# Optimization experiments

Hardware: AMD Instinct MI355X
Metric: run time of the kernel (lower is better)

The kernel has to match this reference:

```python
import jax, jax.numpy as jnp
import numpy as np

B, T, N, IN, H, K = 8, 10, 50, 6, 256, 4
E = N * (N - 1)


def setup_inputs() -> dict:
    key = jax.random.key(0)
    ks = jax.random.split(key, 22)
    p = lambda k, shape: jax.random.normal(k, shape, jnp.float32) * 0.05
    return {
        "inputs": jax.random.normal(ks[0], (B, T, N, IN), jnp.float32),
        "sampled_edges": jax.random.uniform(ks[1], (B, T, E, K), dtype=jnp.float32),
        "msg_w1": p(ks[2], (K, H, 2 * H)), "msg_b1": p(ks[3], (K, H)),
        "msg_w2": p(ks[4], (K, H, H)), "msg_b2": p(ks[5], (K, H)),
        "w_hr": p(ks[6], (H, H)), "w_hi": p(ks[7], (H, H)), "w_hh": p(ks[8], (H, H)),
        "w_ir": p(ks[9], (H, IN)), "b_ir": p(ks[10], (H,)),
        "w_ii": p(ks[11], (H, IN)), "b_ii": p(ks[12], (H,)),
        "w_in": p(ks[13], (H, IN)), "b_in": p(ks[14], (H,)),
        "w_o1": p(ks[15], (H, H)), "b_o1": p(ks[16], (H,)),
        "w_o2": p(ks[17], (H, H)), "b_o2": p(ks[18], (H,)),
        "w_o3": p(ks[19], (IN, H)), "b_o3": p(ks[20], (IN,)),
    }


def reference(inputs, sampled_edges, msg_w1, msg_b1, msg_w2, msg_b2,
              w_hr, w_hi, w_hh, w_ir, b_ir, w_ii, b_ii, w_in, b_in,
              w_o1, b_o1, w_o2, b_o2, w_o3, b_o3):
    b, t, n, _ = inputs.shape
    k = msg_w1.shape[0]
    h = msg_w1.shape[1]
    # fully-connected directed graph, no self loops (static indices)
    send_np, recv_np = np.where(np.ones((n, n)) - np.eye(n))
    send = jnp.asarray(send_np)
    recv = jnp.asarray(recv_np)
    norm = float(k) - 1.0  # skip_first_edge_type = True

    def single_step(ins, rel, hidden):
        # ins: [B,N,IN], rel: [B,E,K], hidden: [B,N,H]
        pre = jnp.concatenate([hidden[:, recv], hidden[:, send]], axis=-1)  # [B,E,2H]
        all_msgs = jnp.zeros((b, pre.shape[1], h), inputs.dtype)
        for i in range(1, k):  # skip first edge type
            m = jnp.tanh(jnp.einsum('bef,hf->beh', pre, msg_w1[i]) + msg_b1[i])
            m = jnp.tanh(jnp.einsum('beh,jh->bej', m, msg_w2[i]) + msg_b2[i])
            all_msgs = all_msgs + m * rel[:, :, i:i + 1] / norm
        # scatter-add messages to receiver nodes (replaces onehot matmul)
        agg = jnp.zeros((b, n, h), inputs.dtype).at[:, recv].add(all_msgs) / (n - 1)
        r = jax.nn.sigmoid(ins @ w_ir.T + b_ir + agg @ w_hr.T)
        ig = jax.nn.sigmoid(ins @ w_ii.T + b_ii + agg @ w_hi.T)
        nn_ = jnp.tanh(ins @ w_in.T + b_in + r * (agg @ w_hh.T))
        hidden = (1 - ig) * nn_ + ig * hidden
        pred = jax.nn.relu(hidden @ w_o1.T + b_o1)
        pred = jax.nn.relu(pred @ w_o2.T + b_o2)
        pred = ins + (pred @ w_o3.T + b_o3)
        return pred, hidden

    x_t = jnp.swapaxes(inputs, 0, 1)         # [T,B,N,IN]
    e_t = jnp.swapaxes(sampled_edges, 0, 1)  # [T,B,E,K]
    h0 = jnp.zeros((b, n, h), inputs.dtype)

    def step(carry, xs):
        hidden, prev = carry
        xt, et, s = xs
        ins = jnp.where(s == 0, xt, prev)  # teacher_forcing=False: only step 0 uses inputs
        pred, hidden = single_step(ins, et, hidden)
        return (hidden, pred), pred

    _, preds = jax.lax.scan(step, (h0, jnp.zeros_like(x_t[0])), (x_t, e_t, jnp.arange(t)))
    return jnp.swapaxes(preds, 0, 1)  # [B,T,N,IN]
```

## Files before the change

### kernel.cpp

```cpp
#include <hip/hip_runtime.h>
#include <hip/hip_bf16.h>
#include <stdint.h>

#define B_ 8
#define T_ 10
#define N_ 50
#define IN_ 6
#define H_ 256
#define K_ 4
#define E_ 2450
#define ROWS 400
#define AP 102400

typedef __attribute__((ext_vector_type(8))) __bf16 bf16x8;
typedef __attribute__((ext_vector_type(4))) float f32x4;

__device__ __forceinline__ unsigned short f2bf(float x) {
    unsigned int u = __float_as_uint(x);
    u = (u + 0x7fffu + ((u >> 16) & 1u)) >> 16;
    return (unsigned short)u;
}
__device__ __forceinline__ unsigned pk2(float a, float b) {
    return (unsigned)f2bf(a) | ((unsigned)f2bf(b) << 16);
}
__device__ __forceinline__ float rcp_fast(float x) { return __builtin_amdgcn_rcpf(x); }
__device__ __forceinline__ float tanh_fast(float x) {
    float e = __expf(2.0f * x);
    return 1.0f - 2.0f * rcp_fast(e + 1.0f);
}
__device__ __forceinline__ float sigmoid_fast(float x) {
    return rcp_fast(1.0f + __expf(-x));
}

__global__ __launch_bounds__(256) void swizzle_weights(
        const float* __restrict__ w1, const float* __restrict__ w2,
        const float* __restrict__ whr, const float* __restrict__ whi,
        const float* __restrict__ whh, const float* __restrict__ wo1,
        const float* __restrict__ wo2,
        unsigned short* __restrict__ w1s, unsigned short* __restrict__ w2s,
        unsigned short* __restrict__ gws, unsigned short* __restrict__ wos,
        unsigned int* __restrict__ zero_region) {
    const int W1N = 3 * 16 * 16 * 64 * 8;
    const int W2N = 3 * 16 * 8 * 64 * 8;
    const int GWN = 3 * 65536;
    const int WON = 2 * 65536;
    int idx = blockIdx.x * 256 + threadIdx.x;
    if (idx < W1N) {
        int j = idx & 7, L = (idx >> 3) & 63, kt = (idx >> 9) & 15;
        int nt = (idx >> 13) & 15, i = idx >> 17;
        int n = nt * 16 + (L & 15);
        int k = kt * 32 + ((L >> 4) << 3) + j;
        w1s[idx] = f2bf(w1[((size_t)(i + 1) * H_ + n) * (2 * H_) + k]);
    } else if (idx < W1N + W2N) {
        int t = idx - W1N;
        int j = t & 7, L = (t >> 3) & 63, kt = (t >> 9) & 7;
        int nt = (t >> 12) & 15, i = t >> 16;
        int n = nt * 16 + (L & 15);
        int k = kt * 32 + ((L >> 4) << 3) + j;
        w2s[t] = f2bf(w2[((size_t)(i + 1) * H_ + n) * H_ + k]);
    } else if (idx < W1N + W2N + GWN) {
        int t = idx - (W1N + W2N);
        int j = t & 7, L = (t >> 3) & 63, kt = (t >> 9) & 7;
        int nt = (t >> 12) & 15, mat = t >> 16;
        int n = nt * 16 + (L & 15);
        int k = kt * 32 + ((L >> 4) << 3) + j;
        const float* src = (mat == 0) ? whr : (mat == 1) ? whi : whh;
        gws[t] = f2bf(src[(size_t)n * H_ + k]);
    } else if (idx < W1N + W2N + GWN + WON) {
        int t = idx - (W1N + W2N + GWN);
        int j = t & 7, L = (t >> 3) & 63, kt = (t >> 9) & 7;
        int nt = (t >> 12) & 15, g = t >> 16;
        int n = nt * 16 + (L & 15);
        int k = kt * 32 + ((L >> 4) << 3) + j;
        const float* src = (g == 0) ? wo1 : wo2;
        wos[t] = f2bf(src[(size_t)n * H_ + k]);
    } else {
        int t = idx - (W1N + W2N + GWN + WON);
        if (t < 153600) zero_region[t] = 0u;
    }
}

__global__ __launch_bounds__(256) void uv_kernel(
        const unsigned short* __restrict__ hb, const unsigned short* __restrict__ w1s,
        const float* __restrict__ b1, float* __restrict__ UV) {
    int mm = blockIdx.x / 6;
    int tyh = blockIdx.x % 6;
    int ty = tyh >> 1, half = tyh & 1;
    int lane = threadIdx.x & 63, wid = threadIdx.x >> 6;
    int col = lane & 15, q = lane >> 4;
    const bf16x8* w1f = (const bf16x8*)w1s;

    f32x4 acc[4];
    #pragma unroll
    for (int u = 0; u < 4; ++u) acc[u] = (f32x4){0.f, 0.f, 0.f, 0.f};
    #pragma unroll
    for (int kt = 0; kt < 8; ++kt) {
        bf16x8 a = *(const bf16x8*)&hb[(size_t)(mm * 16 + col) * H_ + kt * 32 + q * 8];
        #pragma unroll
        for (int u = 0; u < 4; ++u) {
            bf16x8 w = w1f[(size_t)((ty * 16 + wid * 4 + u) * 16 + half * 8 + kt) * 64 + lane];
            acc[u] = __builtin_amdgcn_mfma_f32_16x16x32_bf16(a, w, acc[u], 0, 0, 0);
        }
    }
    #pragma unroll
    for (int u = 0; u < 4; ++u) {
        float bias = (half == 0) ? b1[(ty + 1) * H_ + (wid * 4 + u) * 16 + col] : 0.0f;
        #pragma unroll
        for (int r = 0; r < 4; ++r)
            UV[((size_t)(mm * 16 + q * 4 + r) * 3 + ty) * 512 + half * 256 +
               (wid * 4 + u) * 16 + col] = acc[u][r] + bias;
    }
}

__global__ __launch_bounds__(256, 4) void msgagg_kernel(
        const float* __restrict__ UV, const float* __restrict__ edges,
        const unsigned short* __restrict__ w2s,
        const float* __restrict__ b2, float* __restrict__ aggP, int t) {
    __shared__ unsigned short m1F[32 * 512];
    __shared__ float relS[64];

    int ty = blockIdx.x / 400;
    int rem = blockIdx.x - ty * 400;
    int b = rem / 50;
    int r = rem - b * 50;
    int tid = threadIdx.x;
    int lane = tid & 63, wid = tid >> 6;
    int col = lane & 15, q = lane >> 4;

    if (tid < 64) {
        float v = 0.0f;
        if (tid < 50 && tid != r) {
            int e = tid * 49 + (r > tid ? r - 1 : r);
            v = edges[(((size_t)b * T_ + t) * E_ + e) * K_ + ty + 1];
        }
        relS[tid] = v;
    }

    {
        int row = wid * 16 + col;
        int sv = row < N_ ? row : N_ - 1;
        float fl = (row < N_) ? 1.0f : 0.0f;
        const float* Vrow = &UV[((size_t)(b * N_ + sv) * 3 + ty) * 512 + 256 + q * 8];
        const float* Urow = &UV[((size_t)(b * N_ + r) * 3 + ty) * 512 + q * 8];
        #pragma unroll
        for (int kt = 0; kt < 8; ++kt) {
            float4 v0 = *(const float4*)(Vrow + kt * 32);
            float4 v1 = *(const float4*)(Vrow + kt * 32 + 4);
            float4 u0 = *(const float4*)(Urow + kt * 32);
            float4 u1 = *(const float4*)(Urow + kt * 32 + 4);
            float m0 = tanh_fast(u0.x + v0.x) * fl;
            float m1 = tanh_fast(u0.y + v0.y) * fl;
            float m2 = tanh_fast(u0.z + v0.z) * fl;
            float m3 = tanh_fast(u0.w + v0.w) * fl;
            float m4 = tanh_fast(u1.x + v1.x) * fl;
            float m5 = tanh_fast(u1.y + v1.y) * fl;
            float m6 = tanh_fast(u1.z + v1.z) * fl;
            float m7 = tanh_fast(u1.w + v1.w) * fl;
            uint4 pk;
            pk.x = pk2(m0, m1); pk.y = pk2(m2, m3);
            pk.z = pk2(m4, m5); pk.w = pk2(m6, m7);
            *(uint4*)&m1F[(wid * 8 + kt) * 512 + lane * 8] = pk;
        }
    }
    __syncthreads();

    const bf16x8* w2f = (const bf16x8*)w2s;
    f32x4 acc[4][4];
    #pragma unroll
    for (int mt = 0; mt < 4; ++mt)
        #pragma unroll
        for (int u = 0; u < 4; ++u) acc[mt][u] = (f32x4){0.f, 0.f, 0.f, 0.f};

    #pragma unroll
    for (int kt = 0; kt < 8; ++kt) {
        bf16x8 a0 = *(const bf16x8*)&m1F[(0 * 8 + kt) * 512 + lane * 8];
        bf16x8 a1 = *(const bf16x8*)&m1F[(1 * 8 + kt) * 512 + lane * 8];
        bf16x8 a2 = *(const bf16x8*)&m1F[(2 * 8 + kt) * 512 + lane * 8];
        bf16x8 a3 = *(const bf16x8*)&m1F[(3 * 8 + kt) * 512 + lane * 8];
        #pragma unroll
        for (int u = 0; u < 4; ++u) {
            bf16x8 w = w2f[(size_t)((ty * 16 + wid * 4 + u) * 8 + kt) * 64 + lane];
            acc[0][u] = __builtin_amdgcn_mfma_f32_16x16x32_bf16(a0, w, acc[0][u], 0, 0, 0);
            acc[1][u] = __builtin_amdgcn_mfma_f32_16x16x32_bf16(a1, w, acc[1][u], 0, 0, 0);
            acc[2][u] = __builtin_amdgcn_mfma_f32_16x16x32_bf16(a2, w, acc[2][u], 0, 0, 0);
            acc[3][u] = __builtin_amdgcn_mfma_f32_16x16x32_bf16(a3, w, acc[3][u], 0, 0, 0);
        }
    }
    #pragma unroll
    for (int u = 0; u < 4; ++u) {
        float bias = b2[(ty + 1) * H_ + (wid * 4 + u) * 16 + col];
        float sum = 0.0f;
        #pragma unroll
        for (int mt = 0; mt < 4; ++mt)
            #pragma unroll
            for (int rg = 0; rg < 4; ++rg) {
                int row = mt * 16 + q * 4 + rg;
                sum += tanh_fast(acc[mt][u][rg] + bias) * relS[row];
            }
        sum += __shfl_xor(sum, 16);
        sum += __shfl_xor(sum, 32);
        if (lane < 16)
            aggP[(size_t)ty * AP + (size_t)(b * N_ + r) * H_ +
                 (wid * 4 + u) * 16 + col] = sum * (1.0f / 147.0f);
    }
}

__global__ __launch_bounds__(256) void node_kernel(
        const float* __restrict__ inputs, const float* __restrict__ aggP,
        const unsigned short* __restrict__ gws, const unsigned short* __restrict__ wos,
        float* __restrict__ hidden, unsigned short* __restrict__ hidden_bf,
        const float* __restrict__ w_ir, const float* __restrict__ b_ir,
        const float* __restrict__ w_ii, const float* __restrict__ b_ii,
        const float* __restrict__ w_in, const float* __restrict__ b_in,
        const float* __restrict__ b_o1, const float* __restrict__ b_o2,
        const float* __restrict__ w_o3, const float* __restrict__ b_o3,
        float* __restrict__ out, int t) {
    __shared__ unsigned short aggF[8 * 512];
    __shared__ unsigned short hnF[8 * 512];
    __shared__ unsigned short p1F[8 * 512];
    __shared__ float p2L[16 * 260];
    __shared__ float insS[16 * 6];

    int mm = blockIdx.x;
    int tid = threadIdx.x;
    int lane = tid & 63, wid = tid >> 6;
    int col = lane & 15, q = lane >> 4;

    const float* src = (t == 0) ? inputs : out;
    int tt = (t == 0) ? 0 : (t - 1);

    #pragma unroll
    for (int s = 0; s < 2; ++s) {
        int slot = tid + s * 256;
        int kt = slot >> 6, L = slot & 63;
        int row = mm * 16 + (L & 15);
        int k0 = kt * 32 + ((L >> 4) << 3);
        const float* p = &aggP[(size_t)row * H_ + k0];
        float4 a0 = *(const float4*)(p);
        float4 a1 = *(const float4*)(p + 4);
        float4 b0 = *(const float4*)(p + AP);
        float4 b1 = *(const float4*)(p + AP + 4);
        float4 c0 = *(const float4*)(p + 2 * AP);
        float4 c1 = *(const float4*)(p + 2 * AP + 4);
        uint4 pk;
        pk.x = pk2(a0.x + b0.x + c0.x, a0.y + b0.y + c0.y);
        pk.y = pk2(a0.z + b0.z + c0.z, a0.w + b0.w + c0.w);
        pk.z = pk2(a1.x + b1.x + c1.x, a1.y + b1.y + c1.y);
        pk.w = pk2(a1.z + b1.z + c1.z, a1.w + b1.w + c1.w);
        *(uint4*)&aggF[(size_t)kt * 512 + L * 8] = pk;
    }
    if (tid < 96) {
        int rl = tid / 6, c = tid - rl * 6;
        int row = mm * 16 + rl;
        int b = row / 50, n = row - b * 50;
        insS[rl * 6 + c] = src[(((size_t)b * T_ + tt) * N_ + n) * IN_ + c];
    }
    __syncthreads();

    const bf16x8* gwf = (const bf16x8*)gws;
    f32x4 acc[3][4];
    #pragma unroll
    for (int m = 0; m < 3; ++m)
        #pragma unroll
        for (int u = 0; u < 4; ++u) acc[m][u] = (f32x4){0.f, 0.f, 0.f, 0.f};
    #pragma unroll
    for (int kt = 0; kt < 8; ++kt) {
        bf16x8 a = *(const bf16x8*)&aggF[kt * 512 + lane * 8];
        #pragma unroll
        for (int m = 0; m < 3; ++m)
            #pragma unroll
            for (int u = 0; u < 4; ++u) {
                bf16x8 w = gwf[(size_t)((m * 16 + wid * 4 + u) * 8 + kt) * 64 + lane];
                acc[m][u] = __builtin_amdgcn_mfma_f32_16x16x32_bf16(a, w, acc[m][u], 0, 0, 0);
            }
    }

    #pragma unroll
    for (int u = 0; u < 4; ++u) {
        int h = (wid * 4 + u) * 16 + col;
        float bir = b_ir[h], bii = b_ii[h], bin_ = b_in[h];
        float wir[6], wii[6], win[6];
        #pragma unroll
        for (int c = 0; c < 6; ++c) {
            wir[c] = w_ir[h * 6 + c];
            wii[c] = w_ii[h * 6 + c];
            win[c] = w_in[h * 6 + c];
        }
        #pragma unroll
        for (int rg = 0; rg < 4; ++rg) {
            int rl = q * 4 + rg;
            int row = mm * 16 + rl;
            float xr = bir, xi = bii, xn = bin_;
            #pragma unroll
            for (int c = 0; c < 6; ++c) {
                float iv = insS[rl * 6 + c];
                xr += wir[c] * iv;
                xi += wii[c] * iv;
                xn += win[c] * iv;
            }
            float rgate = sigmoid_fast(xr + acc[0][u][rg]);
            float igate = sigmoid_fast(xi + acc[1][u][rg]);
            float nn = tanh_fast(xn + rgate * acc[2][u][rg]);
            size_t off = (size_t)row * H_ + h;
            float hold = hidden[off];
            float hnew = (1.0f - igate) * nn + igate * hold;
            hidden[off] = hnew;
            hidden_bf[off] = f2bf(hnew);
            hnF[(h >> 5) * 512 + (((h >> 3) & 3) * 16 + rl) * 8 + (h & 7)] = f2bf(hnew);
        }
    }
    __syncthreads();

    const bf16x8* wof = (const bf16x8*)wos;
    f32x4 a1v[4];
    #pragma unroll
    for (int u = 0; u < 4; ++u) a1v[u] = (f32x4){0.f, 0.f, 0.f, 0.f};
    #pragma unroll
    for (int kt = 0; kt < 8; ++kt) {
        bf16x8 a = *(const bf16x8*)&hnF[kt * 512 + lane * 8];
        #pragma unroll
        for (int u = 0; u < 4; ++u) {
            bf16x8 w = wof[(size_t)((wid * 4 + u) * 8 + kt) * 64 + lane];
            a1v[u] = __builtin_amdgcn_mfma_f32_16x16x32_bf16(a, w, a1v[u], 0, 0, 0);
        }
    }
    #pragma unroll
    for (int u = 0; u < 4; ++u) {
        int h = (wid * 4 + u) * 16 + col;
        float bo = b_o1[h];
        #pragma unroll
        for (int rg = 0; rg < 4; ++rg) {
            int rl = q * 4 + rg;
            float v = fmaxf(a1v[u][rg] + bo, 0.0f);
            p1F[(h >> 5) * 512 + (((h >> 3) & 3) * 16 + rl) * 8 + (h & 7)] = f2bf(v);
        }
    }
    __syncthreads();

    f32x4 a2v[4];
    #pragma unroll
    for (int u = 0; u < 4; ++u) a2v[u] = (f32x4){0.f, 0.f, 0.f, 0.f};
    #pragma unroll
    for (int kt = 0; kt < 8; ++kt) {
        bf16x8 a = *(const bf16x8*)&p1F[kt * 512 + lane * 8];
        #pragma unroll
        for (int u = 0; u < 4; ++u) {
            bf16x8 w = wof[(size_t)((16 + wid * 4 + u) * 8 + kt) * 64 + lane];
            a2v[u] = __builtin_amdgcn_mfma_f32_16x16x32_bf16(a, w, a2v[u], 0, 0, 0);
        }
    }
    #pragma unroll
    for (int u = 0; u < 4; ++u) {
        int h = (wid * 4 + u) * 16 + col;
        float bo = b_o2[h];
        #pragma unroll
        for (int rg = 0; rg < 4; ++rg) {
            int rl = q * 4 + rg;
            p2L[rl * 260 + h] = fmaxf(a2v[u][rg] + bo, 0.0f);
        }
    }
    __syncthreads();

    if (tid < 96) {
        int rl = tid / 6, c = tid - rl * 6;
        int row = mm * 16 + rl;
        float acc3 = b_o3[c];
        for (int k = 0; k < 256; k += 4) {
            float4 w = *(const float4*)&w_o3[c * 256 + k];
            float4 p = *(const float4*)&p2L[rl * 260 + k];
            acc3 += w.x * p.x + w.y * p.y + w.z * p.z + w.w * p.w;
        }
        int b = row / 50, n = row - b * 50;
        out[(((size_t)b * T_ + t) * N_ + n) * IN_ + c] = insS[rl * 6 + c] + acc3;
    }
}

extern "C" void kernel_launch(void* const* d_in, const int* in_sizes, int n_in,
                              void* d_out, int out_size, void* d_ws, size_t ws_size,
                              hipStream_t stream) {
    const float* inputs = (const float*)d_in[0];
    const float* edges  = (const float*)d_in[1];
    const float* msg_w1 = (const float*)d_in[2];
    const float* msg_b1 = (const float*)d_in[3];
    const float* msg_w2 = (const float*)d_in[4];
    const float* msg_b2 = (const float*)d_in[5];
    const float* w_hr = (const float*)d_in[6];
    const float* w_hi = (const float*)d_in[7];
    const float* w_hh = (const float*)d_in[8];
    const float* w_ir = (const float*)d_in[9];
    const float* b_ir = (const float*)d_in[10];
    const float* w_ii = (const float*)d_in[11];
    const float* b_ii = (const float*)d_in[12];
    const float* w_in = (const float*)d_in[13];
    const float* b_in = (const float*)d_in[14];
    const float* w_o1 = (const float*)d_in[15];
    const float* b_o1 = (const float*)d_in[16];
    const float* w_o2 = (const float*)d_in[17];
    const float* b_o2 = (const float*)d_in[18];
    const float* w_o3 = (const float*)d_in[19];
    const float* b_o3 = (const float*)d_in[20];
    float* out = (float*)d_out;

    char* ws = (char*)d_ws;
    float* hidden            = (float*)(ws);
    unsigned short* hidden_bf= (unsigned short*)(ws + 409600);
    float* UV                = (float*)(ws + 614400);
    float* aggP              = (float*)(ws + 3072000);
    unsigned short* w1s      = (unsigned short*)(ws + 4300800);
    unsigned short* w2s      = (unsigned short*)(ws + 5087232);
    unsigned short* gws      = (unsigned short*)(ws + 5480448);
    unsigned short* wos      = (unsigned short*)(ws + 5873664);

    swizzle_weights<<<dim3(4184), dim3(256), 0, stream>>>(
        msg_w1, msg_w2, w_hr, w_hi, w_hh, w_o1, w_o2, w1s, w2s, gws, wos,
        (unsigned int*)ws);

    for (int t = 0; t < T_; ++t) {
        uv_kernel<<<dim3(150), dim3(256), 0, stream>>>(hidden_bf, w1s, msg_b1, UV);
        msgagg_kernel<<<dim3(1200), dim3(256), 0, stream>>>(
            UV, edges, w2s, msg_b2, aggP, t);
        node_kernel<<<dim3(25), dim3(256), 0, stream>>>(
            inputs, aggP, gws, wos, hidden, hidden_bf,
            w_ir, b_ir, w_ii, b_ii, w_in, b_in, b_o1, b_o2, w_o3, b_o3, out, t);
    }
}
```

Measured before the change: 590.8 us.

## Fuse per-step UV projection into node kernel and drop uv_kernel launch

The separate uv_kernel, which projected the hidden state through msg_w1 each step, is removed. The UV projection for the next step is now computed at the end of node_kernel from the bf16 hidden tile already in shared memory, and the initial UV is set to the bias because the starting hidden state is zero. This saves one launch per timestep plus the hidden_bf round trip through global memory. In exchange, only 25 blocks now do the whole UV matmul, serially per wave, which lengthens node_kernel. The output projection is also split across two threads per output, and the row mask in msgagg is dropped since relS already zeroes padded rows.

```diff
diff --git a/kernel.cpp b/kernel.cpp
--- a/kernel.cpp
+++ b/kernel.cpp
@@ -36,14 +36,15 @@
         const float* __restrict__ w1, const float* __restrict__ w2,
         const float* __restrict__ whr, const float* __restrict__ whi,
         const float* __restrict__ whh, const float* __restrict__ wo1,
-        const float* __restrict__ wo2,
+        const float* __restrict__ wo2, const float* __restrict__ b1,
         unsigned short* __restrict__ w1s, unsigned short* __restrict__ w2s,
         unsigned short* __restrict__ gws, unsigned short* __restrict__ wos,
-        unsigned int* __restrict__ zero_region) {
+        unsigned int* __restrict__ zero_region, float* __restrict__ UV) {
     const int W1N = 3 * 16 * 16 * 64 * 8;
     const int W2N = 3 * 16 * 8 * 64 * 8;
     const int GWN = 3 * 65536;
     const int WON = 2 * 65536;
+    const int ZN  = 102400;
     int idx = blockIdx.x * 256 + threadIdx.x;
     if (idx < W1N) {
         int j = idx & 7, L = (idx >> 3) & 63, kt = (idx >> 9) & 15;
@@ -74,41 +75,13 @@
         int k = kt * 32 + ((L >> 4) << 3) + j;
         const float* src = (g == 0) ? wo1 : wo2;
         wos[t] = f2bf(src[(size_t)n * H_ + k]);
+    } else if (idx < W1N + W2N + GWN + WON + ZN) {
+        zero_region[idx - (W1N + W2N + GWN + WON)] = 0u;
     } else {
-        int t = idx - (W1N + W2N + GWN + WON);
-        if (t < 153600) zero_region[t] = 0u;
-    }
-}
-
-__global__ __launch_bounds__(256) void uv_kernel(
-        const unsigned short* __restrict__ hb, const unsigned short* __restrict__ w1s,
-        const float* __restrict__ b1, float* __restrict__ UV) {
-    int mm = blockIdx.x / 6;
-    int tyh = blockIdx.x % 6;
-    int ty = tyh >> 1, half = tyh & 1;
-    int lane = threadIdx.x & 63, wid = threadIdx.x >> 6;
-    int col = lane & 15, q = lane >> 4;
-    const bf16x8* w1f = (const bf16x8*)w1s;
-
-    f32x4 acc[4];
-    #pragma unroll
-    for (int u = 0; u < 4; ++u) acc[u] = (f32x4){0.f, 0.f, 0.f, 0.f};
-    #pragma unroll
-    for (int kt = 0; kt < 8; ++kt) {
-        bf16x8 a = *(const bf16x8*)&hb[(size_t)(mm * 16 + col) * H_ + kt * 32 + q * 8];
-        #pragma unroll
-        for (int u = 0; u < 4; ++u) {
-            bf16x8 w = w1f[(size_t)((ty * 16 + wid * 4 + u) * 16 + half * 8 + kt) * 64 + lane];
-            acc[u] = __builtin_amdgcn_mfma_f32_16x16x32_bf16(a, w, acc[u], 0, 0, 0);
-        }
-    }
-    #pragma unroll
-    for (int u = 0; u < 4; ++u) {
-        float bias = (half == 0) ? b1[(ty + 1) * H_ + (wid * 4 + u) * 16 + col] : 0.0f;
-        #pragma unroll
-        for (int r = 0; r < 4; ++r)
-            UV[((size_t)(mm * 16 + q * 4 + r) * 3 + ty) * 512 + half * 256 +
-               (wid * 4 + u) * 16 + col] = acc[u][r] + bias;
+        int t = idx - (W1N + W2N + GWN + WON + ZN);
+        int c = t & 511;
+        int ty = (t >> 9) % 3;
+        UV[t] = (c < 256) ? b1[(ty + 1) * H_ + c] : 0.0f;
     }
 }
 
@@ -139,7 +112,6 @@
     {
         int row = wid * 16 + col;
         int sv = row < N_ ? row : N_ - 1;
-        float fl = (row < N_) ? 1.0f : 0.0f;
         const float* Vrow = &UV[((size_t)(b * N_ + sv) * 3 + ty) * 512 + 256 + q * 8];
         const float* Urow = &UV[((size_t)(b * N_ + r) * 3 + ty) * 512 + q * 8];
         #pragma unroll
@@ -148,14 +120,14 @@
             float4 v1 = *(const float4*)(Vrow + kt * 32 + 4);
             float4 u0 = *(const float4*)(Urow + kt * 32);
             float4 u1 = *(const float4*)(Urow + kt * 32 + 4);
-            float m0 = tanh_fast(u0.x + v0.x) * fl;
-            float m1 = tanh_fast(u0.y + v0.y) * fl;
-            float m2 = tanh_fast(u0.z + v0.z) * fl;
-            float m3 = tanh_fast(u0.w + v0.w) * fl;
-            float m4 = tanh_fast(u1.x + v1.x) * fl;
-            float m5 = tanh_fast(u1.y + v1.y) * fl;
-            float m6 = tanh_fast(u1.z + v1.z) * fl;
-            float m7 = tanh_fast(u1.w + v1.w) * fl;
+            float m0 = tanh_fast(u0.x + v0.x);
+            float m1 = tanh_fast(u0.y + v0.y);
+            float m2 = tanh_fast(u0.z + v0.z);
+            float m3 = tanh_fast(u0.w + v0.w);
+            float m4 = tanh_fast(u1.x + v1.x);
+            float m5 = tanh_fast(u1.y + v1.y);
+            float m6 = tanh_fast(u1.z + v1.z);
+            float m7 = tanh_fast(u1.w + v1.w);
             uint4 pk;
             pk.x = pk2(m0, m1); pk.y = pk2(m2, m3);
             pk.z = pk2(m4, m5); pk.w = pk2(m6, m7);
@@ -208,10 +180,12 @@
 __global__ __launch_bounds__(256) void node_kernel(
         const float* __restrict__ inputs, const float* __restrict__ aggP,
         const unsigned short* __restrict__ gws, const unsigned short* __restrict__ wos,
-        float* __restrict__ hidden, unsigned short* __restrict__ hidden_bf,
+        const unsigned short* __restrict__ w1s,
+        float* __restrict__ hidden, float* __restrict__ UV,
         const float* __restrict__ w_ir, const float* __restrict__ b_ir,
         const float* __restrict__ w_ii, const float* __restrict__ b_ii,
         const float* __restrict__ w_in, const float* __restrict__ b_in,
+        const float* __restrict__ b1,
         const float* __restrict__ b_o1, const float* __restrict__ b_o2,
         const float* __restrict__ w_o3, const float* __restrict__ b_o3,
         float* __restrict__ out, int t) {
@@ -239,14 +213,14 @@
         float4 a0 = *(const float4*)(p);
         float4 a1 = *(const float4*)(p + 4);
         float4 b0 = *(const float4*)(p + AP);
-        float4 b1 = *(const float4*)(p + AP + 4);
+        float4 b1v = *(const float4*)(p + AP + 4);
         float4 c0 = *(const float4*)(p + 2 * AP);
         float4 c1 = *(const float4*)(p + 2 * AP + 4);
         uint4 pk;
         pk.x = pk2(a0.x + b0.x + c0.x, a0.y + b0.y + c0.y);
         pk.y = pk2(a0.z + b0.z + c0.z, a0.w + b0.w + c0.w);
-        pk.z = pk2(a1.x + b1.x + c1.x, a1.y + b1.y + c1.y);
-        pk.w = pk2(a1.z + b1.z + c1.z, a1.w + b1.w + c1.w);
+        pk.z = pk2(a1.x + b1v.x + c1.x, a1.y + b1v.y + c1.y);
+        pk.w = pk2(a1.z + b1v.z + c1.z, a1.w + b1v.w + c1.w);
         *(uint4*)&aggF[(size_t)kt * 512 + L * 8] = pk;
     }
     if (tid < 96) {
@@ -305,7 +279,6 @@
             float hold = hidden[off];
             float hnew = (1.0f - igate) * nn + igate * hold;
             hidden[off] = hnew;
-            hidden_bf[off] = f2bf(hnew);
             hnF[(h >> 5) * 512 + (((h >> 3) & 3) * 16 + rl) * 8 + (h & 7)] = f2bf(hnew);
         }
     }
@@ -361,17 +334,51 @@
     }
     __syncthreads();
 
-    if (tid < 96) {
-        int rl = tid / 6, c = tid - rl * 6;
-        int row = mm * 16 + rl;
-        float acc3 = b_o3[c];
-        for (int k = 0; k < 256; k += 4) {
-            float4 w = *(const float4*)&w_o3[c * 256 + k];
-            float4 p = *(const float4*)&p2L[rl * 260 + k];
+    {
+        const bf16x8* w1f = (const bf16x8*)w1s;
+        bf16x8 af[8];
+        #pragma unroll
+        for (int kt = 0; kt < 8; ++kt)
+            af[kt] = *(const bf16x8*)&hnF[kt * 512 + lane * 8];
+        #pragma unroll
+        for (int gg = 0; gg < 24; ++gg) {
+            int g = wid * 24 + gg;
+            int ty = g >> 5, half = (g >> 4) & 1, nt = g & 15;
+            f32x4 uacc = (f32x4){0.f, 0.f, 0.f, 0.f};
+            #pragma unroll
+            for (int kt = 0; kt < 8; ++kt) {
+                bf16x8 w = w1f[(size_t)((ty * 16 + nt) * 16 + half * 8 + kt) * 64 + lane];
+                uacc = __builtin_amdgcn_mfma_f32_16x16x32_bf16(af[kt], w, uacc, 0, 0, 0);
+            }
+            float bias = (half == 0) ? b1[(ty + 1) * H_ + nt * 16 + col] : 0.0f;
+            #pragma unroll
+            for (int rg = 0; rg < 4; ++rg) {
+                int row = mm * 16 + q * 4 + rg;
+                UV[((size_t)row * 3 + ty) * 512 + half * 256 + nt * 16 + col] =
+                    uacc[rg] + bias;
+            }
+        }
+    }
+
+    if (tid < 192) {
+        int o = tid >> 1;
+        int rl = o / 6, c = o - rl * 6;
+        int half = tid & 1;
+        float acc3 = half ? 0.0f : b_o3[c];
+        const float* wrow = &w_o3[c * 256 + half * 128];
+        const float* prow = &p2L[rl * 260 + half * 128];
+        #pragma unroll
+        for (int k = 0; k < 128; k += 4) {
+            float4 w = *(const float4*)&wrow[k];
+            float4 p = *(const float4*)&prow[k];
             acc3 += w.x * p.x + w.y * p.y + w.z * p.z + w.w * p.w;
         }
-        int b = row / 50, n = row - b * 50;
-        out[(((size_t)b * T_ + t) * N_ + n) * IN_ + c] = insS[rl * 6 + c] + acc3;
+        acc3 += __shfl_xor(acc3, 1);
+        if (!half) {
+            int row = mm * 16 + rl;
+            int b = row / 50, n = row - b * 50;
+            out[(((size_t)b * T_ + t) * N_ + n) * IN_ + c] = insS[rl * 6 + c] + acc3;
+        }
     }
 }
 
@@ -403,7 +410,6 @@
 
     char* ws = (char*)d_ws;
     float* hidden            = (float*)(ws);
-    unsigned short* hidden_bf= (unsigned short*)(ws + 409600);
     float* UV                = (float*)(ws + 614400);
     float* aggP              = (float*)(ws + 3072000);
     unsigned short* w1s      = (unsigned short*)(ws + 4300800);
@@ -411,16 +417,16 @@
     unsigned short* gws      = (unsigned short*)(ws + 5480448);
     unsigned short* wos      = (unsigned short*)(ws + 5873664);
 
-    swizzle_weights<<<dim3(4184), dim3(256), 0, stream>>>(
-        msg_w1, msg_w2, w_hr, w_hi, w_hh, w_o1, w_o2, w1s, w2s, gws, wos,
-        (unsigned int*)ws);
+    swizzle_weights<<<dim3(6384), dim3(256), 0, stream>>>(
+        msg_w1, msg_w2, w_hr, w_hi, w_hh, w_o1, w_o2, msg_b1,
+        w1s, w2s, gws, wos, (unsigned int*)hidden, UV);
 
     for (int t = 0; t < T_; ++t) {
-        uv_kernel<<<dim3(150), dim3(256), 0, stream>>>(hidden_bf, w1s, msg_b1, UV);
         msgagg_kernel<<<dim3(1200), dim3(256), 0, stream>>>(
             UV, edges, w2s, msg_b2, aggP, t);
         node_kernel<<<dim3(25), dim3(256), 0, stream>>>(
-            inputs, aggP, gws, wos, hidden, hidden_bf,
-            w_ir, b_ir, w_ii, b_ii, w_in, b_in, b_o1, b_o2, w_o3, b_o3, out, t);
-    }
-}
+            inputs, aggP, gws, wos, w1s, hidden, UV,
+            w_ir, b_ir, w_ii, b_ii, w_in, b_in, msg_b1,
+            b_o1, b_o2, w_o3, b_o3, out, t);
+    }
+}
```

Measured after the change: 623.9 us. 5.6% more time.

## Split node kernel into 4-row blocks and parallelize output projection reduction

Applied to the files above, without the earlier changes.

The GRU/output node kernel now runs on 100 blocks of 4 rows each instead of 25 blocks of 16 rows, spreading the serial per-step node work over more compute units. The 4 real rows are replicated across the 16-row MFMA tile, and only the first copy is written back, so each block does redundant matrix work. The final 256-wide output dot product is split across 8 lanes and combined with shuffle reductions. The padding-row mask multiply in the message kernel is also removed, relying on the zero edge weights for padded rows.

```diff
diff --git a/kernel.cpp b/kernel.cpp
--- a/kernel.cpp
+++ b/kernel.cpp
@@ -139,7 +139,6 @@
     {
         int row = wid * 16 + col;
         int sv = row < N_ ? row : N_ - 1;
-        float fl = (row < N_) ? 1.0f : 0.0f;
         const float* Vrow = &UV[((size_t)(b * N_ + sv) * 3 + ty) * 512 + 256 + q * 8];
         const float* Urow = &UV[((size_t)(b * N_ + r) * 3 + ty) * 512 + q * 8];
         #pragma unroll
@@ -148,14 +147,14 @@
             float4 v1 = *(const float4*)(Vrow + kt * 32 + 4);
             float4 u0 = *(const float4*)(Urow + kt * 32);
             float4 u1 = *(const float4*)(Urow + kt * 32 + 4);
-            float m0 = tanh_fast(u0.x + v0.x) * fl;
-            float m1 = tanh_fast(u0.y + v0.y) * fl;
-            float m2 = tanh_fast(u0.z + v0.z) * fl;
-            float m3 = tanh_fast(u0.w + v0.w) * fl;
-            float m4 = tanh_fast(u1.x + v1.x) * fl;
-            float m5 = tanh_fast(u1.y + v1.y) * fl;
-            float m6 = tanh_fast(u1.z + v1.z) * fl;
-            float m7 = tanh_fast(u1.w + v1.w) * fl;
+            float m0 = tanh_fast(u0.x + v0.x);
+            float m1 = tanh_fast(u0.y + v0.y);
+            float m2 = tanh_fast(u0.z + v0.z);
+            float m3 = tanh_fast(u0.w + v0.w);
+            float m4 = tanh_fast(u1.x + v1.x);
+            float m5 = tanh_fast(u1.y + v1.y);
+            float m6 = tanh_fast(u1.z + v1.z);
+            float m7 = tanh_fast(u1.w + v1.w);
             uint4 pk;
             pk.x = pk2(m0, m1); pk.y = pk2(m2, m3);
             pk.z = pk2(m4, m5); pk.w = pk2(m6, m7);
@@ -219,7 +218,7 @@
     __shared__ unsigned short hnF[8 * 512];
     __shared__ unsigned short p1F[8 * 512];
     __shared__ float p2L[16 * 260];
-    __shared__ float insS[16 * 6];
+    __shared__ float insS[4 * 6];
 
     int mm = blockIdx.x;
     int tid = threadIdx.x;
@@ -233,25 +232,25 @@
     for (int s = 0; s < 2; ++s) {
         int slot = tid + s * 256;
         int kt = slot >> 6, L = slot & 63;
-        int row = mm * 16 + (L & 15);
+        int row = mm * 4 + (L & 3);
         int k0 = kt * 32 + ((L >> 4) << 3);
         const float* p = &aggP[(size_t)row * H_ + k0];
         float4 a0 = *(const float4*)(p);
         float4 a1 = *(const float4*)(p + 4);
         float4 b0 = *(const float4*)(p + AP);
-        float4 b1 = *(const float4*)(p + AP + 4);
+        float4 b1v = *(const float4*)(p + AP + 4);
         float4 c0 = *(const float4*)(p + 2 * AP);
         float4 c1 = *(const float4*)(p + 2 * AP + 4);
         uint4 pk;
         pk.x = pk2(a0.x + b0.x + c0.x, a0.y + b0.y + c0.y);
         pk.y = pk2(a0.z + b0.z + c0.z, a0.w + b0.w + c0.w);
-        pk.z = pk2(a1.x + b1.x + c1.x, a1.y + b1.y + c1.y);
-        pk.w = pk2(a1.z + b1.z + c1.z, a1.w + b1.w + c1.w);
+        pk.z = pk2(a1.x + b1v.x + c1.x, a1.y + b1v.y + c1.y);
+        pk.w = pk2(a1.z + b1v.z + c1.z, a1.w + b1v.w + c1.w);
         *(uint4*)&aggF[(size_t)kt * 512 + L * 8] = pk;
     }
-    if (tid < 96) {
+    if (tid < 24) {
         int rl = tid / 6, c = tid - rl * 6;
-        int row = mm * 16 + rl;
+        int row = mm * 4 + rl;
         int b = row / 50, n = row - b * 50;
         insS[rl * 6 + c] = src[(((size_t)b * T_ + tt) * N_ + n) * IN_ + c];
     }
@@ -289,11 +288,11 @@
         #pragma unroll
         for (int rg = 0; rg < 4; ++rg) {
             int rl = q * 4 + rg;
-            int row = mm * 16 + rl;
+            int row = mm * 4 + (rl & 3);
             float xr = bir, xi = bii, xn = bin_;
             #pragma unroll
             for (int c = 0; c < 6; ++c) {
-                float iv = insS[rl * 6 + c];
+                float iv = insS[(rl & 3) * 6 + c];
                 xr += wir[c] * iv;
                 xi += wii[c] * iv;
                 xn += win[c] * iv;
@@ -304,8 +303,10 @@
             size_t off = (size_t)row * H_ + h;
             float hold = hidden[off];
             float hnew = (1.0f - igate) * nn + igate * hold;
-            hidden[off] = hnew;
-            hidden_bf[off] = f2bf(hnew);
+            if (rl < 4) {
+                hidden[off] = hnew;
+                hidden_bf[off] = f2bf(hnew);
+            }
             hnF[(h >> 5) * 512 + (((h >> 3) & 3) * 16 + rl) * 8 + (h & 7)] = f2bf(hnew);
         }
     }
@@ -361,17 +362,27 @@
     }
     __syncthreads();
 
-    if (tid < 96) {
-        int rl = tid / 6, c = tid - rl * 6;
-        int row = mm * 16 + rl;
-        float acc3 = b_o3[c];
-        for (int k = 0; k < 256; k += 4) {
-            float4 w = *(const float4*)&w_o3[c * 256 + k];
-            float4 p = *(const float4*)&p2L[rl * 260 + k];
+    if (tid < 192) {
+        int o = tid >> 3;
+        int rl = o / 6, c = o - rl * 6;
+        int part = tid & 7;
+        float acc3 = (part == 0) ? b_o3[c] : 0.0f;
+        const float* wrow = &w_o3[c * 256 + part * 32];
+        const float* prow = &p2L[rl * 260 + part * 32];
+        #pragma unroll
+        for (int k = 0; k < 32; k += 4) {
+            float4 w = *(const float4*)&wrow[k];
+            float4 p = *(const float4*)&prow[k];
             acc3 += w.x * p.x + w.y * p.y + w.z * p.z + w.w * p.w;
         }
-        int b = row / 50, n = row - b * 50;
-        out[(((size_t)b * T_ + t) * N_ + n) * IN_ + c] = insS[rl * 6 + c] + acc3;
+        acc3 += __shfl_xor(acc3, 1);
+        acc3 += __shfl_xor(acc3, 2);
+        acc3 += __shfl_xor(acc3, 4);
+        if (part == 0) {
+            int row = mm * 4 + rl;
+            int b = row / 50, n = row - b * 50;
+            out[(((size_t)b * T_ + t) * N_ + n) * IN_ + c] = insS[rl * 6 + c] + acc3;
+        }
     }
 }
 
@@ -419,7 +430,7 @@
         uv_kernel<<<dim3(150), dim3(256), 0, stream>>>(hidden_bf, w1s, msg_b1, UV);
         msgagg_kernel<<<dim3(1200), dim3(256), 0, stream>>>(
             UV, edges, w2s, msg_b2, aggP, t);
-        node_kernel<<<dim3(25), dim3(256), 0, stream>>>(
+        node_kernel<<<dim3(100), dim3(256), 0, stream>>>(
             inputs, aggP, gws, wos, hidden, hidden_bf,
             w_ir, b_ir, w_ii, b_ii, w_in, b_in, b_o1, b_o2, w_o3, b_o3, out, t);
     }
```

Result: slower. 673.3 us (+14.0%).
